# Kernel optimization log

Hardware: AMD Instinct MI355X
Metric: run time of the kernel (lower is better)

## Reference

```python
import jax, jax.numpy as jnp
import numpy as np

ALPHA = 0.9   # synaptic decay
BETA = 0.8    # membrane decay
THRESH = 1.0  # snntorch default threshold, reset_mechanism='subtract'
DIMS = [7200, 3600, 1800, 900, 450]
B, T, IN_DIM, K = 128, 16, 14400, 25


def setup_inputs() -> dict:
    key = jax.random.key(0)
    ks = jax.random.split(key, 24)
    inp = {}
    inp["x"] = jax.random.normal(ks[0], (B, T, IN_DIM), jnp.float32)
    prev = IN_DIM
    for i, d in enumerate(DIMS):
        inp[f"w{i}"] = jax.random.normal(ks[1 + i], (d, K), jnp.float32) * (2.0 / K) ** 0.5
        inp[f"b{i}"] = jax.random.normal(ks[7 + i], (d,), jnp.float32) * 0.01
        inp[f"knn{i}"] = jax.random.randint(ks[13 + i], (d, K), 0, prev)
        prev = d
    inp["fc_w"] = jax.random.normal(ks[20], (2, DIMS[-1]), jnp.float32) * 0.05
    inp["fc_b"] = jax.random.normal(ks[21], (2,), jnp.float32) * 0.01
    return inp


def _forward(x, ws, bs, knns, fc_w, fc_b):
    n_layer = len(DIMS)

    def lif(inp, syn, mem):
        # snntorch Synaptic, reset_mechanism='subtract': reset computed from
        # the PREVIOUS membrane potential and detached from the graph.
        reset = jax.lax.stop_gradient((mem > THRESH).astype(inp.dtype))
        syn = ALPHA * syn + inp
        mem = BETA * mem + syn - reset * THRESH
        return syn, mem

    def step(carry, xt):
        syns, mems = carry
        h = xt  # (B, prev_dim)
        new_syns, new_mems = [], []
        for i in range(n_layer):
            g = jnp.take(h, knns[i], axis=1)                 # (B, d_i, K) KNN gather
            pre = jnp.einsum('bdk,dk->bd', g, ws[i]) + bs[i]  # weighted sum over K
            syn, mem = lif(pre, syns[i], mems[i])
            new_syns.append(syn)
            new_mems.append(mem)
            h = mem  # module propagates membrane potential to next layer
        angle = h @ fc_w.T + fc_b  # (B, 2)
        return (tuple(new_syns), tuple(new_mems)), angle

    bsz = x.shape[0]
    syns0 = tuple(jnp.zeros((bsz, d), x.dtype) for d in DIMS)
    mems0 = tuple(jnp.zeros((bsz, d), x.dtype) for d in DIMS)
    _, angles = jax.lax.scan(step, (syns0, mems0), jnp.transpose(x, (1, 0, 2)))
    return angles[-1]  # only the final timestep's angle is returned


def reference(x, w0, w1, w2, w3, w4, b0, b1, b2, b3, b4,
              knn0, knn1, knn2, knn3, knn4, fc_w, fc_b):
    return _forward(x, (w0, w1, w2, w3, w4), (b0, b1, b2, b3, b4),
                    (knn0, knn1, knn2, knn3, knn4), fc_w, fc_b)
```

## Files before the change

kernel.cpp:

```cpp
#include <hip/hip_runtime.h>

#define ALPHA 0.9f
#define BETA  0.8f
#define K     25
#define B     128
#define T     16
#define IN_DIM 14400
#define NSL   8
#define SW    16

using u16 = unsigned short;

static __device__ __forceinline__ u16 f2bf(float f) {
  union { float f; unsigned u; } c; c.f = f;
  const unsigned r = c.u + 0x7FFFu + ((c.u >> 16) & 1u);
  return (u16)(r >> 16);
}
static __device__ __forceinline__ float bf2f(u16 h) {
  union { unsigned u; float f; } c; c.u = ((unsigned)h) << 16;
  return c.f;
}

__global__ __launch_bounds__(256) void transpose_bf_kernel(
    const float* __restrict__ x, u16* __restrict__ xTh, int t0) {
  __shared__ float tile[64][65];
  const int tl = blockIdx.z;
  const int t  = t0 + tl;
  const int i0 = blockIdx.x * 64;
  const int b0 = blockIdx.y * 64;
  const int tid = threadIdx.x;

  const int fi = (tid & 15) * 4;
  const int bi = tid >> 4;
#pragma unroll
  for (int p = 0; p < 4; ++p) {
    const int b = bi + p * 16;
    const float4 v = *(const float4*)&x[(size_t)(b0 + b) * (T * IN_DIM) +
                                        (size_t)t * IN_DIM + i0 + fi];
    tile[fi + 0][b] = v.x;
    tile[fi + 1][b] = v.y;
    tile[fi + 2][b] = v.z;
    tile[fi + 3][b] = v.w;
  }
  __syncthreads();
  const int bq = (tid & 15) * 4;
  const int fr = tid >> 4;
  const int e  = (b0 + bq) >> 4;
  const int bl = bq & 15;
#pragma unroll
  for (int p = 0; p < 4; ++p) {
    const int f = fr + p * 16;
    ushort4 v;
    v.x = f2bf(tile[f][bq + 0]);
    v.y = f2bf(tile[f][bq + 1]);
    v.z = f2bf(tile[f][bq + 2]);
    v.w = f2bf(tile[f][bq + 3]);
    *(ushort4*)&xTh[(((size_t)(tl >> 1) * NSL + e) * IN_DIM + (i0 + f)) * 32 +
                    (tl & 1) * SW + bl] = v;
  }
}

template <int NTP, int NPASS>
__global__ __launch_bounds__(256, 4) void lcn_pair_bf(
    const u16* __restrict__ hsrc, const float* __restrict__ w,
    const float* __restrict__ bias, const int* __restrict__ knn,
    u16* __restrict__ memout, float* __restrict__ state,
    int dim, int dprev, int nblk, int load_state, int save_state) {
  const int e    = blockIdx.x & 7;
  const int blk  = blockIdx.x >> 3;
  const int nl   = threadIdx.x >> 3;
  const int l8   = threadIdx.x & 7;
  const int half = l8 >> 2;
  const int bq   = (l8 & 3) * 4;

#pragma unroll 1
  for (int p = 0; p < NPASS; ++p) {
    const int dd = (blk + p * nblk) * 32 + nl;
    const bool act = dd < dim;
    const int d = act ? dd : dim - 1;

    int   idx[K];
    float wr[K];
#pragma unroll
    for (int k = 0; k < K; ++k) {
      idx[k] = knn[d * K + k] * 32 + half * SW + bq;
      wr[k]  = w[d * K + k];
    }
    const float bi = bias[d];

    float4 s = make_float4(0.f, 0.f, 0.f, 0.f);
    float4 m = make_float4(0.f, 0.f, 0.f, 0.f);
    if (load_state) {
      const size_t so = ((size_t)e * dim + d) * SW + bq;
      s = *(const float4*)&state[so];
      m = *(const float4*)&state[(size_t)NSL * dim * SW + so];
    }

    for (int tp = 0; tp < NTP; ++tp) {
      const u16* hp = hsrc + ((size_t)tp * NSL + e) * dprev * 32;
      ushort4 hv[13], hw[12];
#pragma unroll
      for (int j = 0; j < 13; ++j)
        hv[j] = *(const ushort4*)&hp[idx[j]];
#pragma unroll
      for (int j = 0; j < 12; ++j)
        hw[j] = *(const ushort4*)&hp[idx[13 + j]];
      float4 a0 = make_float4(bi, bi, bi, bi);
      float4 a1 = make_float4(0.f, 0.f, 0.f, 0.f);
#pragma unroll
      for (int j = 0; j < 13; ++j) {
        const float wk = wr[j];
        if (j & 1) {
          a1.x = fmaf(wk, bf2f(hv[j].x), a1.x);
          a1.y = fmaf(wk, bf2f(hv[j].y), a1.y);
          a1.z = fmaf(wk, bf2f(hv[j].z), a1.z);
          a1.w = fmaf(wk, bf2f(hv[j].w), a1.w);
        } else {
          a0.x = fmaf(wk, bf2f(hv[j].x), a0.x);
          a0.y = fmaf(wk, bf2f(hv[j].y), a0.y);
          a0.z = fmaf(wk, bf2f(hv[j].z), a0.z);
          a0.w = fmaf(wk, bf2f(hv[j].w), a0.w);
        }
      }
#pragma unroll
      for (int j = 0; j < 12; ++j) {
        const float wk = wr[13 + j];
        if (j & 1) {
          a1.x = fmaf(wk, bf2f(hw[j].x), a1.x);
          a1.y = fmaf(wk, bf2f(hw[j].y), a1.y);
          a1.z = fmaf(wk, bf2f(hw[j].z), a1.z);
          a1.w = fmaf(wk, bf2f(hw[j].w), a1.w);
        } else {
          a0.x = fmaf(wk, bf2f(hw[j].x), a0.x);
          a0.y = fmaf(wk, bf2f(hw[j].y), a0.y);
          a0.z = fmaf(wk, bf2f(hw[j].z), a0.z);
          a0.w = fmaf(wk, bf2f(hw[j].w), a0.w);
        }
      }
      float4 acc;
      acc.x = a0.x + a1.x;
      acc.y = a0.y + a1.y;
      acc.z = a0.z + a1.z;
      acc.w = a0.w + a1.w;
      float4 oth;
      oth.x = __shfl_xor(acc.x, 4, 64);
      oth.y = __shfl_xor(acc.y, 4, 64);
      oth.z = __shfl_xor(acc.z, 4, 64);
      oth.w = __shfl_xor(acc.w, 4, 64);
      const float4 pre0 = half ? oth : acc;
      const float4 pre1 = half ? acc : oth;
      s.x = ALPHA * s.x + pre0.x;
      s.y = ALPHA * s.y + pre0.y;
      s.z = ALPHA * s.z + pre0.z;
      s.w = ALPHA * s.w + pre0.w;
      float4 meven;
      meven.x = BETA * m.x + s.x - ((m.x > 1.0f) ? 1.0f : 0.0f);
      meven.y = BETA * m.y + s.y - ((m.y > 1.0f) ? 1.0f : 0.0f);
      meven.z = BETA * m.z + s.z - ((m.z > 1.0f) ? 1.0f : 0.0f);
      meven.w = BETA * m.w + s.w - ((m.w > 1.0f) ? 1.0f : 0.0f);
      s.x = ALPHA * s.x + pre1.x;
      s.y = ALPHA * s.y + pre1.y;
      s.z = ALPHA * s.z + pre1.z;
      s.w = ALPHA * s.w + pre1.w;
      m.x = BETA * meven.x + s.x - ((meven.x > 1.0f) ? 1.0f : 0.0f);
      m.y = BETA * meven.y + s.y - ((meven.y > 1.0f) ? 1.0f : 0.0f);
      m.z = BETA * meven.z + s.z - ((meven.z > 1.0f) ? 1.0f : 0.0f);
      m.w = BETA * meven.w + s.w - ((meven.w > 1.0f) ? 1.0f : 0.0f);
      if (act) {
        const float4 wv = half ? m : meven;
        ushort4 ov;
        ov.x = f2bf(wv.x);
        ov.y = f2bf(wv.y);
        ov.z = f2bf(wv.z);
        ov.w = f2bf(wv.w);
        *(ushort4*)&memout[(((size_t)tp * NSL + e) * dim + d) * 32 +
                           half * SW + bq] = ov;
      }
    }

    if (save_state && act && half == 0) {
      const size_t so = ((size_t)e * dim + d) * SW + bq;
      *(float4*)&state[so] = s;
      *(float4*)&state[(size_t)NSL * dim * SW + so] = m;
    }
  }
}

__global__ __launch_bounds__(128) void fc_kernel(
    const u16* __restrict__ mem4, const float* __restrict__ fc_w,
    const float* __restrict__ fc_b, float* __restrict__ out) {
  const int b  = threadIdx.x;
  const int e  = b >> 4;
  const int bl = b & 15;
  float a0 = fc_b[0], a1 = fc_b[1];
  const u16* base = mem4 + ((size_t)7 * NSL + e) * 450 * 32;
  for (int d = 0; d < 450; ++d) {
    const float h = bf2f(base[(size_t)d * 32 + SW + bl]);
    a0 += fc_w[d] * h;
    a1 += fc_w[450 + d] * h;
  }
  out[b * 2 + 0] = a0;
  out[b * 2 + 1] = a1;
}

extern "C" void kernel_launch(void* const* d_in, const int* in_sizes, int n_in,
                              void* d_out, int out_size, void* d_ws,
                              size_t ws_size, hipStream_t stream) {
  (void)in_sizes; (void)n_in; (void)out_size; (void)ws_size;
  const float* x = (const float*)d_in[0];
  const float* w[5];
  const float* bias[5];
  const int* knn[5];
  for (int i = 0; i < 5; ++i) {
    w[i]    = (const float*)d_in[1 + 3 * i];
    bias[i] = (const float*)d_in[2 + 3 * i];
    knn[i]  = (const int*)d_in[3 + 3 * i];
  }
  const float* fc_w = (const float*)d_in[16];
  const float* fc_b = (const float*)d_in[17];
  float* out = (float*)d_out;

  static const int DIMS[5] = {7200, 3600, 1800, 900, 450};

  u16* A  = (u16*)d_ws;
  u16* XB = A + 14745600;
  float* S = (float*)(XB + 14745600);

  u16* mem0 = A;
  u16* mem1 = XB;
  u16* mem2 = A;
  u16* mem3 = XB + 7372800;
  u16* mem4 = A;

  for (int stage = 0; stage < 2; ++stage) {
    const int t0 = stage * 8;
    transpose_bf_kernel<<<dim3(IN_DIM / 64, B / 64, 8), 256, 0, stream>>>(
        x, XB, t0);
    lcn_pair_bf<4, 2><<<113 * NSL, 256, 0, stream>>>(
        XB, w[0], bias[0], knn[0], mem0 + (size_t)stage * 7372800, S,
        DIMS[0], IN_DIM, 113, stage, stage == 0);
  }

  static const int NBLK[5] = {113, 113, 57, 29, 15};
  const u16* src = mem0;
  u16* dsts[4] = {mem1, mem2, mem3, mem4};
  for (int i = 1; i < 5; ++i) {
    lcn_pair_bf<8, 1><<<NBLK[i] * NSL, 256, 0, stream>>>(
        src, w[i], bias[i], knn[i], dsts[i - 1], nullptr, DIMS[i],
        DIMS[i - 1], NBLK[i], 0, 0);
    src = dsts[i - 1];
  }

  fc_kernel<<<1, 128, 0, stream>>>(mem4, fc_w, fc_b, out);
}
```

Before: 344.8 us.

## Pin transpose blocks to batch slices with persistent tiles matching the LCN layout

Replaces the grid-wide 64x64 transpose with a persistent kernel of 1024 blocks. The block index is split as blockIdx & 7 for the slice and blockIdx >> 3 for the slot, the same split the LCN kernel uses. This is apparently meant to keep each slice's converted data in the L2/cache partition of the blocks that later read it. Each tile covers 16 batch rows times a time pair times 96 features, so every output write is a full contiguous 32-element bf16 row. The risks are fewer blocks in flight and two barriers per tile loop iteration, which could limit memory parallelism.

```diff
diff --git a/kernel.cpp b/kernel.cpp
--- a/kernel.cpp
+++ b/kernel.cpp
@@ -8,6 +8,8 @@
 #define IN_DIM 14400
 #define NSL   8
 #define SW    16
+#define CF    96
+#define NCH   150
 
 using u16 = unsigned short;
 
@@ -21,42 +23,46 @@
   return c.f;
 }
 
-__global__ __launch_bounds__(256) void transpose_bf_kernel(
-    const float* __restrict__ x, u16* __restrict__ xTh, int t0) {
-  __shared__ float tile[64][65];
-  const int tl = blockIdx.z;
-  const int t  = t0 + tl;
-  const int i0 = blockIdx.x * 64;
-  const int b0 = blockIdx.y * 64;
-  const int tid = threadIdx.x;
-
-  const int fi = (tid & 15) * 4;
-  const int bi = tid >> 4;
-#pragma unroll
-  for (int p = 0; p < 4; ++p) {
-    const int b = bi + p * 16;
-    const float4 v = *(const float4*)&x[(size_t)(b0 + b) * (T * IN_DIM) +
-                                        (size_t)t * IN_DIM + i0 + fi];
-    tile[fi + 0][b] = v.x;
-    tile[fi + 1][b] = v.y;
-    tile[fi + 2][b] = v.z;
-    tile[fi + 3][b] = v.w;
-  }
-  __syncthreads();
-  const int bq = (tid & 15) * 4;
-  const int fr = tid >> 4;
-  const int e  = (b0 + bq) >> 4;
-  const int bl = bq & 15;
-#pragma unroll
-  for (int p = 0; p < 4; ++p) {
-    const int f = fr + p * 16;
-    ushort4 v;
-    v.x = f2bf(tile[f][bq + 0]);
-    v.y = f2bf(tile[f][bq + 1]);
-    v.z = f2bf(tile[f][bq + 2]);
-    v.w = f2bf(tile[f][bq + 3]);
-    *(ushort4*)&xTh[(((size_t)(tl >> 1) * NSL + e) * IN_DIM + (i0 + f)) * 32 +
-                    (tl & 1) * SW + bl] = v;
+__global__ __launch_bounds__(256, 4) void transpose_pair_pinned(
+    const float* __restrict__ x, u16* __restrict__ xTh, int t0, int slots) {
+  __shared__ float lds[CF][33];
+  const int e    = blockIdx.x & 7;
+  const int slot = blockIdx.x >> 3;
+  const int tid  = threadIdx.x;
+  const int rid  = tid >> 3;
+  const int fq   = tid & 7;
+  const int tpar = rid >> 4;
+  const int bl   = rid & 15;
+  const int b    = e * 16 + bl;
+
+  const int ntiles = 4 * NCH;
+  for (int ti = slot; ti < ntiles; ti += slots) {
+    const int tp = ti / NCH;
+    const int ch = ti - tp * NCH;
+    const int i0 = ch * CF;
+    const int t  = t0 + tp * 2 + tpar;
+    const float* xr = x + ((size_t)b * T + t) * IN_DIM + i0;
+#pragma unroll
+    for (int pf = 0; pf < CF / 32; ++pf) {
+      const float4 v = *(const float4*)&xr[pf * 32 + fq * 4];
+      lds[pf * 32 + fq * 4 + 0][rid] = v.x;
+      lds[pf * 32 + fq * 4 + 1][rid] = v.y;
+      lds[pf * 32 + fq * 4 + 2][rid] = v.z;
+      lds[pf * 32 + fq * 4 + 3][rid] = v.w;
+    }
+    __syncthreads();
+#pragma unroll
+    for (int wp = 0; wp < CF / 32; ++wp) {
+      const int f = wp * 32 + rid;
+      ushort4 ov;
+      ov.x = f2bf(lds[f][fq * 4 + 0]);
+      ov.y = f2bf(lds[f][fq * 4 + 1]);
+      ov.z = f2bf(lds[f][fq * 4 + 2]);
+      ov.w = f2bf(lds[f][fq * 4 + 3]);
+      *(ushort4*)&xTh[(((size_t)tp * NSL + e) * IN_DIM + (i0 + f)) * 32 +
+                      fq * 4] = ov;
+    }
+    __syncthreads();
   }
 }
 
@@ -234,8 +240,7 @@
 
   for (int stage = 0; stage < 2; ++stage) {
     const int t0 = stage * 8;
-    transpose_bf_kernel<<<dim3(IN_DIM / 64, B / 64, 8), 256, 0, stream>>>(
-        x, XB, t0);
+    transpose_pair_pinned<<<128 * NSL, 256, 0, stream>>>(x, XB, t0, 128);
     lcn_pair_bf<4, 2><<<113 * NSL, 256, 0, stream>>>(
         XB, w[0], bias[0], knn[0], mem0 + (size_t)stage * 7372800, S,
         DIMS[0], IN_DIM, 113, stage, stage == 0);
```

Measured after the change: 336.0 us. 1.03x faster.

## Keep layer-0 input in fp32 with per-timestep layout and dedicated kernel

Applied to the files above, without the earlier changes.

The transpose now writes x as fp32 in a 16-wide batch-slice layout, one timestep per slab, instead of pairing two timesteps as bf16. A new layer-0 kernel uses 128 threads, processes one timestep per iteration, splits its gathers into two batches to cut register pressure, and writes into the paired bf16 layout that later layers expect. The workspace now gives each layer its own buffer instead of ping-ponging. Layer-0 input precision improves, but the gathered input traffic doubles (fp32 vs bf16) and there are twice as many serial timestep iterations per thread.

```diff
diff --git a/kernel.cpp b/kernel.cpp
--- a/kernel.cpp
+++ b/kernel.cpp
@@ -8,6 +8,7 @@
 #define IN_DIM 14400
 #define NSL   8
 #define SW    16
+#define NPG   32
 
 using u16 = unsigned short;
 
@@ -21,8 +22,8 @@
   return c.f;
 }
 
-__global__ __launch_bounds__(256) void transpose_bf_kernel(
-    const float* __restrict__ x, u16* __restrict__ xTh, int t0) {
+__global__ __launch_bounds__(256) void transpose_x4_kernel(
+    const float* __restrict__ x, float* __restrict__ xTf, int t0) {
   __shared__ float tile[64][65];
   const int tl = blockIdx.z;
   const int t  = t0 + tl;
@@ -50,13 +51,130 @@
 #pragma unroll
   for (int p = 0; p < 4; ++p) {
     const int f = fr + p * 16;
-    ushort4 v;
-    v.x = f2bf(tile[f][bq + 0]);
-    v.y = f2bf(tile[f][bq + 1]);
-    v.z = f2bf(tile[f][bq + 2]);
-    v.w = f2bf(tile[f][bq + 3]);
-    *(ushort4*)&xTh[(((size_t)(tl >> 1) * NSL + e) * IN_DIM + (i0 + f)) * 32 +
-                    (tl & 1) * SW + bl] = v;
+    float4 v;
+    v.x = tile[f][bq + 0];
+    v.y = tile[f][bq + 1];
+    v.z = tile[f][bq + 2];
+    v.w = tile[f][bq + 3];
+    *(float4*)&xTf[(((size_t)tl * NSL + e) * IN_DIM + (i0 + f)) * SW + bl] = v;
+  }
+}
+
+__global__ __launch_bounds__(128, 4) void lcn0_f32(
+    const float* __restrict__ hsrc, const float* __restrict__ w,
+    const float* __restrict__ bias, const int* __restrict__ knn,
+    u16* __restrict__ memout, float* __restrict__ state,
+    int t0, int load_state, int save_state) {
+  const int e  = blockIdx.x & 7;
+  const int g  = blockIdx.x >> 3;
+  const int nl = threadIdx.x >> 2;
+  const int bq = (threadIdx.x & 3) * 4;
+  const int d  = g * NPG + nl;
+
+  int   idx[K];
+  float wr[K];
+#pragma unroll
+  for (int k = 0; k < K; ++k) {
+    idx[k] = knn[d * K + k] * SW + bq;
+    wr[k]  = w[d * K + k];
+  }
+  const float bi = bias[d];
+
+  float4 sy = make_float4(0.f, 0.f, 0.f, 0.f);
+  float4 me = make_float4(0.f, 0.f, 0.f, 0.f);
+  if (load_state) {
+    const size_t so = ((size_t)e * 7200 + d) * SW + bq;
+    sy = *(const float4*)&state[so];
+    me = *(const float4*)&state[(size_t)NSL * 7200 * SW + so];
+  }
+
+  for (int tl = 0; tl < 8; ++tl) {
+    const float* hp = hsrc + ((size_t)tl * NSL + e) * IN_DIM * SW;
+    float4 ha[9], hb[8];
+#pragma unroll
+    for (int j = 0; j < 8; ++j) ha[j] = *(const float4*)&hp[idx[j]];
+#pragma unroll
+    for (int j = 0; j < 8; ++j) hb[j] = *(const float4*)&hp[idx[8 + j]];
+    float4 a0 = make_float4(bi, bi, bi, bi);
+    float4 a1 = make_float4(0.f, 0.f, 0.f, 0.f);
+#pragma unroll
+    for (int j = 0; j < 8; ++j) {
+      const float wk = wr[j];
+      if (j & 1) {
+        a1.x = fmaf(wk, ha[j].x, a1.x);
+        a1.y = fmaf(wk, ha[j].y, a1.y);
+        a1.z = fmaf(wk, ha[j].z, a1.z);
+        a1.w = fmaf(wk, ha[j].w, a1.w);
+      } else {
+        a0.x = fmaf(wk, ha[j].x, a0.x);
+        a0.y = fmaf(wk, ha[j].y, a0.y);
+        a0.z = fmaf(wk, ha[j].z, a0.z);
+        a0.w = fmaf(wk, ha[j].w, a0.w);
+      }
+    }
+#pragma unroll
+    for (int j = 0; j < 9; ++j) ha[j] = *(const float4*)&hp[idx[16 + j]];
+#pragma unroll
+    for (int j = 0; j < 8; ++j) {
+      const float wk = wr[8 + j];
+      if (j & 1) {
+        a1.x = fmaf(wk, hb[j].x, a1.x);
+        a1.y = fmaf(wk, hb[j].y, a1.y);
+        a1.z = fmaf(wk, hb[j].z, a1.z);
+        a1.w = fmaf(wk, hb[j].w, a1.w);
+      } else {
+        a0.x = fmaf(wk, hb[j].x, a0.x);
+        a0.y = fmaf(wk, hb[j].y, a0.y);
+        a0.z = fmaf(wk, hb[j].z, a0.z);
+        a0.w = fmaf(wk, hb[j].w, a0.w);
+      }
+    }
+#pragma unroll
+    for (int j = 0; j < 9; ++j) {
+      const float wk = wr[16 + j];
+      if (j & 1) {
+        a1.x = fmaf(wk, ha[j].x, a1.x);
+        a1.y = fmaf(wk, ha[j].y, a1.y);
+        a1.z = fmaf(wk, ha[j].z, a1.z);
+        a1.w = fmaf(wk, ha[j].w, a1.w);
+      } else {
+        a0.x = fmaf(wk, ha[j].x, a0.x);
+        a0.y = fmaf(wk, ha[j].y, a0.y);
+        a0.z = fmaf(wk, ha[j].z, a0.z);
+        a0.w = fmaf(wk, ha[j].w, a0.w);
+      }
+    }
+    const float4 acc = make_float4(a0.x + a1.x, a0.y + a1.y, a0.z + a1.z,
+                                   a0.w + a1.w);
+    sy.x = ALPHA * sy.x + acc.x;
+    sy.y = ALPHA * sy.y + acc.y;
+    sy.z = ALPHA * sy.z + acc.z;
+    sy.w = ALPHA * sy.w + acc.w;
+    float4 r;
+    r.x = (me.x > 1.0f) ? 1.0f : 0.0f;
+    r.y = (me.y > 1.0f) ? 1.0f : 0.0f;
+    r.z = (me.z > 1.0f) ? 1.0f : 0.0f;
+    r.w = (me.w > 1.0f) ? 1.0f : 0.0f;
+    me.x = BETA * me.x + sy.x - r.x;
+    me.y = BETA * me.y + sy.y - r.y;
+    me.z = BETA * me.z + sy.z - r.z;
+    me.w = BETA * me.w + sy.w - r.w;
+    const int t   = t0 + tl;
+    const int tp  = t >> 1;
+    const int par = t & 1;
+    ushort4 ov;
+    ov.x = f2bf(me.x);
+    ov.y = f2bf(me.y);
+    ov.z = f2bf(me.z);
+    ov.w = f2bf(me.w);
+    *(ushort4*)&memout[(((size_t)tp * NSL + e) * 7200 + d) * 32 + par * SW +
+                       bq] = ov;
+  }
+
+  if (save_state) {
+    const size_t so = ((size_t)e * 7200 + d) * SW + bq;
+    *(float4*)&state[so] = sy;
+    *(float4*)&state[(size_t)NSL * 7200 * SW + so] = me;
   }
 }
 
@@ -220,36 +338,31 @@
   const float* fc_b = (const float*)d_in[17];
   float* out = (float*)d_out;
 
-  static const int DIMS[5] = {7200, 3600, 1800, 900, 450};
-
-  u16* A  = (u16*)d_ws;
-  u16* XB = A + 14745600;
-  float* S = (float*)(XB + 14745600);
-
-  u16* mem0 = A;
-  u16* mem1 = XB;
-  u16* mem2 = A;
-  u16* mem3 = XB + 7372800;
-  u16* mem4 = A;
+  float* xTf = (float*)d_ws;
+  float* S   = xTf + 14745600;
+  u16* mem0  = (u16*)(S + 1843200);
+  u16* mem1  = mem0 + 14745600;
+  u16* mem2  = mem1 + 7372800;
+  u16* mem3  = mem2 + 3686400;
+  u16* mem4  = mem3 + 1843200;
 
   for (int stage = 0; stage < 2; ++stage) {
     const int t0 = stage * 8;
-    transpose_bf_kernel<<<dim3(IN_DIM / 64, B / 64, 8), 256, 0, stream>>>(
-        x, XB, t0);
-    lcn_pair_bf<4, 2><<<113 * NSL, 256, 0, stream>>>(
-        XB, w[0], bias[0], knn[0], mem0 + (size_t)stage * 7372800, S,
-        DIMS[0], IN_DIM, 113, stage, stage == 0);
-  }
-
-  static const int NBLK[5] = {113, 113, 57, 29, 15};
-  const u16* src = mem0;
-  u16* dsts[4] = {mem1, mem2, mem3, mem4};
-  for (int i = 1; i < 5; ++i) {
-    lcn_pair_bf<8, 1><<<NBLK[i] * NSL, 256, 0, stream>>>(
-        src, w[i], bias[i], knn[i], dsts[i - 1], nullptr, DIMS[i],
-        DIMS[i - 1], NBLK[i], 0, 0);
-    src = dsts[i - 1];
-  }
+    transpose_x4_kernel<<<dim3(IN_DIM / 64, B / 64, 8), 256, 0, stream>>>(
+        x, xTf, t0);
+    lcn0_f32<<<225 * NSL, 128, 0, stream>>>(
+        xTf, w[0], bias[0], knn[0], mem0, S, t0, stage,
+        stage == 0);
+  }
+
+  lcn_pair_bf<8, 1><<<113 * NSL, 256, 0, stream>>>(
+      mem0, w[1], bias[1], knn[1], mem1, nullptr, 3600, 7200, 113, 0, 0);
+  lcn_pair_bf<8, 1><<<57 * NSL, 256, 0, stream>>>(
+      mem1, w[2], bias[2], knn[2], mem2, nullptr, 1800, 3600, 57, 0, 0);
+  lcn_pair_bf<8, 1><<<29 * NSL, 256, 0, stream>>>(
+      mem2, w[3], bias[3], knn[3], mem3, nullptr, 900, 1800, 29, 0, 0);
+  lcn_pair_bf<8, 1><<<15 * NSL, 256, 0, stream>>>(
+      mem3, w[4], bias[4], knn[4], mem4, nullptr, 450, 900, 15, 0, 0);
 
   fc_kernel<<<1, 128, 0, stream>>>(mem4, fc_w, fc_b, out);
 }
```

Result: faster. 329.9 us (median of 2 runs) (-4.3%).
